# Kernel optimization log

Measured on AMD Instinct MI355X. Metric: run time of the kernel, lower is better.

## Reference

```python
import jax, jax.numpy as jnp
import numpy as np

N = 8192
F_IN = 128
F_OUT = 128


def setup_inputs() -> dict:
    key = jax.random.key(0)
    k1, k2, k3, k4, k5 = jax.random.split(key, 5)
    x = jax.random.normal(k1, (N, F_IN), dtype=jnp.float32)
    adj = jax.random.uniform(k2, (N, N), dtype=jnp.float32)
    kernel = jax.random.normal(k3, (F_IN, F_OUT), dtype=jnp.float32) * 0.05
    bias = jax.random.normal(k4, (F_OUT,), dtype=jnp.float32) * 0.05
    beta = jax.random.uniform(k5, (N,), dtype=jnp.float32)
    return {"x": x, "adj": adj, "kernel": kernel, "bias": bias, "beta": beta}


def reference(x, adj, kernel, bias, beta):
    # torch: diag(1/(adj.sum(1)+beta)) @ (adj + diag(beta)) @ x @ kernel + bias
    # (adj + diag(beta)) @ x  ==  adj @ x + beta[:, None] * x  (no NxN temp)
    inv_deg = 1.0 / (jnp.sum(adj, axis=1) + beta)        # [N]
    agg = adj @ x + beta[:, None] * x                     # [N, F_in]
    out = (inv_deg[:, None] * agg) @ kernel + bias        # [N, F_out]
    return out
```

## Files before the change

### kernel.cpp

```cpp
#include <hip/hip_runtime.h>

#define NN 8192
#define FD 128
#define BK 64
#define LDSR 72

typedef float f32x4 __attribute__((ext_vector_type(4)));
typedef short short8 __attribute__((ext_vector_type(8)));
typedef unsigned short ushort4v __attribute__((ext_vector_type(4)));
typedef unsigned short ushort8v __attribute__((ext_vector_type(8)));

__device__ __forceinline__ unsigned short f2bf(float f) {
  unsigned int u = __builtin_bit_cast(unsigned int, f);
  u += 0x7fffu + ((u >> 16) & 1u);
  return (unsigned short)(u >> 16);
}
__device__ __forceinline__ float bf2f(unsigned short h) {
  unsigned int u = ((unsigned int)h) << 16;
  return __builtin_bit_cast(float, u);
}

__global__ __launch_bounds__(256) void xk_kernel(
    const float* __restrict__ x, const float* __restrict__ kern,
    unsigned short* __restrict__ bfrag, unsigned short* __restrict__ xk_rm) {
  __shared__ __align__(16) unsigned short kl[FD * FD];
  __shared__ __align__(16) float xl[16 * FD];
  const int t = threadIdx.x;
  const int row0 = blockIdx.x * 16;

  #pragma unroll
  for (int j = 0; j < 16; ++j) {
    int idx = (j * 256 + t) * 4;
    f32x4 kv = *(const f32x4*)&kern[idx];
    ushort4v kw;
    #pragma unroll
    for (int q = 0; q < 4; ++q) kw[q] = f2bf(kv[q]);
    *(ushort4v*)&kl[idx] = kw;
  }
  #pragma unroll
  for (int j = 0; j < 2; ++j) {
    int idx = (j * 256 + t) * 4;
    *(f32x4*)&xl[idx] = *(const f32x4*)&x[(size_t)row0 * FD + idx];
  }
  __syncthreads();

  const int r0 = (t >> 5) * 2;
  const int c0 = (t & 31) * 4;
  float acc[2][4] = {};
  #pragma unroll 4
  for (int k = 0; k < FD; ++k) {
    ushort4v kq = *(const ushort4v*)&kl[k * FD + c0];
    float kv[4];
    #pragma unroll
    for (int q = 0; q < 4; ++q) kv[q] = bf2f(kq[q]);
    float x0 = xl[r0 * FD + k];
    float x1 = xl[(r0 + 1) * FD + k];
    #pragma unroll
    for (int q = 0; q < 4; ++q) {
      acc[0][q] += x0 * kv[q];
      acc[1][q] += x1 * kv[q];
    }
  }
  #pragma unroll
  for (int i = 0; i < 2; ++i) {
    const int r = row0 + r0 + i;
    const int kt = r >> 5;
    const int lhi = ((r >> 3) & 3) * 16;
    const int j = r & 7;
    ushort4v ow;
    #pragma unroll
    for (int q = 0; q < 4; ++q) {
      const int c = c0 + q;
      unsigned short bv = f2bf(acc[i][q]);
      ow[q] = bv;
      bfrag[(((size_t)kt * 8 + (c >> 4)) * 64 + (lhi + (c & 15))) * 8 + j] = bv;
    }
    *(ushort4v*)&xk_rm[(size_t)r * FD + c0] = ow;
  }
}

template <int S>
__global__ __launch_bounds__(256) void gcn_mm(
    const float* __restrict__ adj, const unsigned short* __restrict__ bfrag,
    unsigned short* __restrict__ parts, float* __restrict__ rowpart) {
  constexpr int KW = NN / S;
  constexpr int NS = KW / BK;
  __shared__ __align__(16) unsigned short sA[4][2][32 * LDSR];

  const int t = threadIdx.x;
  const int l = t & 63;
  const int w = t >> 6;
  const int b = blockIdx.x;
  const int s = b & (S - 1);
  const int row0 = (b / S) * 128 + w * 32;
  const int kbase = s * KW;

  const float* ap = adj + (size_t)(row0 + (l >> 4)) * NN + kbase + (l & 15) * 4;
  unsigned short* sw = &sA[w][0][0];
  const int wofs = (l >> 4) * LDSR + (l & 15) * 4;
  const unsigned short* bp = bfrag + (size_t)l * 8;

  f32x4 Lr[8];
  f32x4 acc[2][8] = {};
  float rs[8] = {0.f, 0.f, 0.f, 0.f, 0.f, 0.f, 0.f, 0.f};

  #pragma unroll
  for (int i = 0; i < 8; ++i)
    Lr[i] = *(const f32x4*)(ap + (size_t)i * 4 * NN);
  #pragma unroll
  for (int i = 0; i < 8; ++i) {
    ushort4v cw;
    #pragma unroll
    for (int q = 0; q < 4; ++q) cw[q] = f2bf(Lr[i][q]);
    rs[i] += Lr[i][0] + Lr[i][1] + Lr[i][2] + Lr[i][3];
    *(ushort4v*)&sw[wofs + i * 4 * LDSR] = cw;
  }

  #pragma unroll 2
  for (int st = 0; st < NS; ++st) {
    const int cur = st & 1;
    if (st + 1 < NS) {
      #pragma unroll
      for (int i = 0; i < 8; ++i)
        Lr[i] = *(const f32x4*)(ap + (size_t)i * 4 * NN + (st + 1) * BK);
    }
    const int ktg = s * (KW / 32) + st * 2;
    #pragma unroll
    for (int h = 0; h < 2; ++h) {
      const int abase = cur * 32 * LDSR + h * 32 + (l >> 4) * 8;
      short8 aF0 = *(const short8*)&sw[abase + (l & 15) * LDSR];
      short8 aF1 = *(const short8*)&sw[abase + (16 + (l & 15)) * LDSR];
      #pragma unroll
      for (int cb = 0; cb < 8; ++cb) {
        ushort8v Bf = *(const ushort8v*)(bp + (((size_t)(ktg + h) * 8 + cb) << 9));
        acc[0][cb] = __builtin_amdgcn_mfma_f32_16x16x32_bf16(aF0, Bf, acc[0][cb], 0, 0, 0);
        acc[1][cb] = __builtin_amdgcn_mfma_f32_16x16x32_bf16(aF1, Bf, acc[1][cb], 0, 0, 0);
      }
    }
    if (st + 1 < NS) {
      const int nb = (cur ^ 1) * 32 * LDSR;
      #pragma unroll
      for (int i = 0; i < 8; ++i) {
        ushort4v cw;
        #pragma unroll
        for (int q = 0; q < 4; ++q) cw[q] = f2bf(Lr[i][q]);
        rs[i] += Lr[i][0] + Lr[i][1] + Lr[i][2] + Lr[i][3];
        *(ushort4v*)&sw[nb + wofs + i * 4 * LDSR] = cw;
      }
    }
  }

  #pragma unroll
  for (int i = 0; i < 8; ++i) {
    rs[i] += __shfl_xor(rs[i], 1);
    rs[i] += __shfl_xor(rs[i], 2);
    rs[i] += __shfl_xor(rs[i], 4);
    rs[i] += __shfl_xor(rs[i], 8);
  }
  if ((l & 15) == 0) {
    #pragma unroll
    for (int i = 0; i < 8; ++i)
      rowpart[(size_t)s * NN + row0 + i * 4 + (l >> 4)] = rs[i];
  }

  unsigned short* pp = parts + ((size_t)s * NN + row0) * FD;
  #pragma unroll
  for (int rf = 0; rf < 2; ++rf)
    #pragma unroll
    for (int cb = 0; cb < 8; ++cb)
      #pragma unroll
      for (int j = 0; j < 4; ++j) {
        const int r = rf * 16 + ((l >> 4) << 2) + j;
        pp[(size_t)r * FD + cb * 16 + (l & 15)] = f2bf(acc[rf][cb][j]);
      }
}

__global__ __launch_bounds__(256) void gcn_fin(
    const unsigned short* __restrict__ parts, const float* __restrict__ rowpart,
    const unsigned short* __restrict__ xk_rm, const float* __restrict__ beta,
    const float* __restrict__ bias, float* __restrict__ out, int S) {
  const int t = threadIdx.x;
  const int r = blockIdx.x * 16 + (t >> 4);
  const int c0 = (t & 15) * 8;

  float rsum = 0.f;
  for (int s = 0; s < S; ++s) rsum += rowpart[(size_t)s * NN + r];
  const float bt = beta[r];
  const float inv = 1.0f / (rsum + bt);

  float a[8] = {0.f, 0.f, 0.f, 0.f, 0.f, 0.f, 0.f, 0.f};
  for (int s = 0; s < S; ++s) {
    ushort8v pv = *(const ushort8v*)&parts[((size_t)s * NN + r) * FD + c0];
    #pragma unroll
    for (int q = 0; q < 8; ++q) a[q] += bf2f(pv[q]);
  }
  ushort8v xv = *(const ushort8v*)&xk_rm[(size_t)r * FD + c0];
  f32x4 o0, o1;
  #pragma unroll
  for (int q = 0; q < 4; ++q) {
    o0[q] = (a[q] + bt * bf2f(xv[q])) * inv + bias[c0 + q];
    o1[q] = (a[4 + q] + bt * bf2f(xv[4 + q])) * inv + bias[c0 + 4 + q];
  }
  *(f32x4*)&out[(size_t)r * FD + c0] = o0;
  *(f32x4*)&out[(size_t)r * FD + c0 + 4] = o1;
}

extern "C" void kernel_launch(void* const* d_in, const int* in_sizes, int n_in,
                              void* d_out, int out_size, void* d_ws, size_t ws_size,
                              hipStream_t stream) {
  const float* x    = (const float*)d_in[0];
  const float* adj  = (const float*)d_in[1];
  const float* kern = (const float*)d_in[2];
  const float* bias = (const float*)d_in[3];
  const float* beta = (const float*)d_in[4];
  float* out = (float*)d_out;

  char* ws = (char*)d_ws;
  unsigned short* bfrag = (unsigned short*)ws;
  unsigned short* xk_rm = (unsigned short*)(ws + (size_t)NN * FD * 2);
  const size_t off_rowpart = (size_t)NN * FD * 4;
  float* rowpart = (float*)(ws + off_rowpart);
  const size_t off_parts = off_rowpart + (size_t)8 * NN * 4;
  unsigned short* parts = (unsigned short*)(ws + off_parts);

  int S = 8;
  while (S > 1 && off_parts + (size_t)S * NN * FD * 2 > ws_size) S >>= 1;

  hipLaunchKernelGGL(xk_kernel, dim3(NN / 16), dim3(256), 0, stream,
                     x, kern, bfrag, xk_rm);

  dim3 blk(256);
  switch (S) {
    case 8: hipLaunchKernelGGL(gcn_mm<8>, dim3(64 * 8), blk, 0, stream, adj, bfrag, parts, rowpart); break;
    case 4: hipLaunchKernelGGL(gcn_mm<4>, dim3(64 * 4), blk, 0, stream, adj, bfrag, parts, rowpart); break;
    case 2: hipLaunchKernelGGL(gcn_mm<2>, dim3(64 * 2), blk, 0, stream, adj, bfrag, parts, rowpart); break;
    default: hipLaunchKernelGGL(gcn_mm<1>, dim3(64), blk, 0, stream, adj, bfrag, parts, rowpart); break;
  }

  hipLaunchKernelGGL(gcn_fin, dim3(NN / 16), dim3(256), 0, stream,
                     parts, rowpart, xk_rm, beta, bias, out, S);
}
```

Measured before the change: 85.15 us.

## Deepen adj prefetch to two stages and batch B-fragment loads in gcn_mm

Restructures the gcn_mm main loop to double-buffer adj tiles in two register sets, so loads are issued two k-steps ahead. It also hoists all B-fragment global loads ahead of the MFMA block, raises wave priority with s_setprio around the MFMAs, and sets launch_bounds(256,2). The aim is to hide HBM latency on the adj stream and keep the matrix cores busy. The extra register arrays raise VGPR pressure and could cost occupancy or cause spills.

```diff
diff --git a/kernel.cpp b/kernel.cpp
--- a/kernel.cpp
+++ b/kernel.cpp
@@ -79,8 +79,47 @@
   }
 }
 
+#define PREFETCH(Lr, stp)                                                     \
+  do {                                                                        \
+    _Pragma("unroll") for (int i = 0; i < 8; ++i)                             \
+        Lr[i] = *(const f32x4*)(ap + (size_t)i * 4 * NN + (stp) * BK);        \
+  } while (0)
+
+#define STAGE(Lr, bufofs)                                                     \
+  do {                                                                        \
+    _Pragma("unroll") for (int i = 0; i < 8; ++i) {                           \
+      ushort4v cw;                                                            \
+      _Pragma("unroll") for (int q = 0; q < 4; ++q) cw[q] = f2bf(Lr[i][q]);   \
+      rs[i] += Lr[i][0] + Lr[i][1] + Lr[i][2] + Lr[i][3];                     \
+      *(ushort4v*)&sw[(bufofs) + wofs + i * 4 * LDSR] = cw;                   \
+    }                                                                         \
+  } while (0)
+
+#define MFMA_STEP(stp, bufofs)                                                \
+  do {                                                                        \
+    const int ktg = kt0 + (stp) * 2;                                          \
+    ushort8v Bf[2][8];                                                        \
+    _Pragma("unroll") for (int h = 0; h < 2; ++h)                             \
+        _Pragma("unroll") for (int cb = 0; cb < 8; ++cb)                      \
+            Bf[h][cb] = *(const ushort8v*)(bp +                               \
+                (((size_t)(ktg + h) * 8 + cb) << 9));                         \
+    __builtin_amdgcn_s_setprio(1);                                            \
+    _Pragma("unroll") for (int h = 0; h < 2; ++h) {                           \
+      const int abase = (bufofs) + h * 32 + (l >> 4) * 8;                     \
+      short8 aF0 = *(const short8*)&sw[abase + (l & 15) * LDSR];              \
+      short8 aF1 = *(const short8*)&sw[abase + (16 + (l & 15)) * LDSR];       \
+      _Pragma("unroll") for (int cb = 0; cb < 8; ++cb) {                      \
+        acc[0][cb] = __builtin_amdgcn_mfma_f32_16x16x32_bf16(                 \
+            aF0, Bf[h][cb], acc[0][cb], 0, 0, 0);                             \
+        acc[1][cb] = __builtin_amdgcn_mfma_f32_16x16x32_bf16(                 \
+            aF1, Bf[h][cb], acc[1][cb], 0, 0, 0);                             \
+      }                                                                       \
+    }                                                                         \
+    __builtin_amdgcn_s_setprio(0);                                            \
+  } while (0)
+
 template <int S>
-__global__ __launch_bounds__(256) void gcn_mm(
+__global__ __launch_bounds__(256, 2) void gcn_mm(
     const float* __restrict__ adj, const unsigned short* __restrict__ bfrag,
     unsigned short* __restrict__ parts, float* __restrict__ rowpart) {
   constexpr int KW = NN / S;
@@ -94,60 +133,29 @@
   const int s = b & (S - 1);
   const int row0 = (b / S) * 128 + w * 32;
   const int kbase = s * KW;
+  const int kt0 = s * (KW / 32);
 
   const float* ap = adj + (size_t)(row0 + (l >> 4)) * NN + kbase + (l & 15) * 4;
   unsigned short* sw = &sA[w][0][0];
   const int wofs = (l >> 4) * LDSR + (l & 15) * 4;
+  const int B1OFS = 32 * LDSR;
   const unsigned short* bp = bfrag + (size_t)l * 8;
 
-  f32x4 Lr[8];
+  f32x4 LrA[8], LrB[8];
   f32x4 acc[2][8] = {};
   float rs[8] = {0.f, 0.f, 0.f, 0.f, 0.f, 0.f, 0.f, 0.f};
 
-  #pragma unroll
-  for (int i = 0; i < 8; ++i)
-    Lr[i] = *(const f32x4*)(ap + (size_t)i * 4 * NN);
-  #pragma unroll
-  for (int i = 0; i < 8; ++i) {
-    ushort4v cw;
-    #pragma unroll
-    for (int q = 0; q < 4; ++q) cw[q] = f2bf(Lr[i][q]);
-    rs[i] += Lr[i][0] + Lr[i][1] + Lr[i][2] + Lr[i][3];
-    *(ushort4v*)&sw[wofs + i * 4 * LDSR] = cw;
-  }
-
-  #pragma unroll 2
-  for (int st = 0; st < NS; ++st) {
-    const int cur = st & 1;
-    if (st + 1 < NS) {
-      #pragma unroll
-      for (int i = 0; i < 8; ++i)
-        Lr[i] = *(const f32x4*)(ap + (size_t)i * 4 * NN + (st + 1) * BK);
-    }
-    const int ktg = s * (KW / 32) + st * 2;
-    #pragma unroll
-    for (int h = 0; h < 2; ++h) {
-      const int abase = cur * 32 * LDSR + h * 32 + (l >> 4) * 8;
-      short8 aF0 = *(const short8*)&sw[abase + (l & 15) * LDSR];
-      short8 aF1 = *(const short8*)&sw[abase + (16 + (l & 15)) * LDSR];
-      #pragma unroll
-      for (int cb = 0; cb < 8; ++cb) {
-        ushort8v Bf = *(const ushort8v*)(bp + (((size_t)(ktg + h) * 8 + cb) << 9));
-        acc[0][cb] = __builtin_amdgcn_mfma_f32_16x16x32_bf16(aF0, Bf, acc[0][cb], 0, 0, 0);
-        acc[1][cb] = __builtin_amdgcn_mfma_f32_16x16x32_bf16(aF1, Bf, acc[1][cb], 0, 0, 0);
-      }
-    }
-    if (st + 1 < NS) {
-      const int nb = (cur ^ 1) * 32 * LDSR;
-      #pragma unroll
-      for (int i = 0; i < 8; ++i) {
-        ushort4v cw;
-        #pragma unroll
-        for (int q = 0; q < 4; ++q) cw[q] = f2bf(Lr[i][q]);
-        rs[i] += Lr[i][0] + Lr[i][1] + Lr[i][2] + Lr[i][3];
-        *(ushort4v*)&sw[nb + wofs + i * 4 * LDSR] = cw;
-      }
-    }
+  PREFETCH(LrA, 0);
+  STAGE(LrA, 0);
+  PREFETCH(LrB, 1);
+
+  for (int st = 0; st < NS; st += 2) {
+    if (st + 2 < NS) PREFETCH(LrA, st + 2);
+    MFMA_STEP(st, 0);
+    STAGE(LrB, B1OFS);
+    if (st + 3 < NS) PREFETCH(LrB, st + 3);
+    MFMA_STEP(st + 1, B1OFS);
+    if (st + 2 < NS) STAGE(LrA, 0);
   }
 
   #pragma unroll
```

Result: faster. 83.40 us (-2.1%).

## Restructure adjacency GEMM into 32-row full-K panels with swizzled LDS and column-split waves

Applied to the files above, without the earlier changes.

Changes gcn_mm so each block loads a whole 32x1024 slice of adj into a swizzled 64KB LDS panel in one pass, instead of streaming 64-wide K tiles per wave with register double-buffering. The four waves then split the 128 output columns, 32 per wave, rather than splitting rows. This gives 2048 blocks with launch_bounds(256,2), trading the per-step load/compute overlap for more parallelism and occupancy. It also fixes the split count at 8 and drops the workspace-size fallback.

```diff
diff --git a/kernel.cpp b/kernel.cpp
--- a/kernel.cpp
+++ b/kernel.cpp
@@ -2,8 +2,10 @@
 
 #define NN 8192
 #define FD 128
-#define BK 64
-#define LDSR 72
+#define RPB 32
+#define SPL 8
+#define KW (NN / SPL)
+#define NKS (KW / 32)
 
 typedef float f32x4 __attribute__((ext_vector_type(4)));
 typedef short short8 __attribute__((ext_vector_type(8)));
@@ -79,117 +81,109 @@
   }
 }
 
-template <int S>
-__global__ __launch_bounds__(256) void gcn_mm(
+__global__ __launch_bounds__(256, 2) void gcn_mm(
     const float* __restrict__ adj, const unsigned short* __restrict__ bfrag,
     unsigned short* __restrict__ parts, float* __restrict__ rowpart) {
-  constexpr int KW = NN / S;
-  constexpr int NS = KW / BK;
-  __shared__ __align__(16) unsigned short sA[4][2][32 * LDSR];
+  __shared__ unsigned short panel[RPB * 1024];
+  __shared__ float rs_l[4][8];
 
   const int t = threadIdx.x;
   const int l = t & 63;
   const int w = t >> 6;
   const int b = blockIdx.x;
-  const int s = b & (S - 1);
-  const int row0 = (b / S) * 128 + w * 32;
+  const int s = b & (SPL - 1);
+  const int row0 = (b >> 3) * RPB;
   const int kbase = s * KW;
-
-  const float* ap = adj + (size_t)(row0 + (l >> 4)) * NN + kbase + (l & 15) * 4;
-  unsigned short* sw = &sA[w][0][0];
-  const int wofs = (l >> 4) * LDSR + (l & 15) * 4;
+  const int kt0 = s * NKS;
+
+  const float* ap = adj + (size_t)row0 * NN + kbase;
+  float rsum[8] = {};
+
+  #pragma unroll
+  for (int half = 0; half < 2; ++half) {
+    f32x4 v[16];
+    #pragma unroll
+    for (int i16 = 0; i16 < 16; ++i16) {
+      const int i = half * 16 + i16;
+      const int rr = i >> 2, ch = i & 3;
+      v[i16] = *(const f32x4*)(ap + (size_t)(w * 8 + rr) * NN + ch * 256 + l * 4);
+    }
+    #pragma unroll
+    for (int i16 = 0; i16 < 16; ++i16) {
+      const int i = half * 16 + i16;
+      const int rr = i >> 2, ch = i & 3;
+      const int row_l = w * 8 + rr;
+      ushort4v cw;
+      #pragma unroll
+      for (int q = 0; q < 4; ++q) cw[q] = f2bf(v[i16][q]);
+      rsum[rr] += v[i16][0] + v[i16][1] + v[i16][2] + v[i16][3];
+      const int unit = (ch * 32 + (l >> 1)) ^ (row_l & 7);
+      *(ushort4v*)&panel[row_l * 1024 + unit * 8 + (l & 1) * 4] = cw;
+    }
+  }
+
+  #pragma unroll
+  for (int rr = 0; rr < 8; ++rr) {
+    rsum[rr] += __shfl_xor(rsum[rr], 1);
+    rsum[rr] += __shfl_xor(rsum[rr], 2);
+    rsum[rr] += __shfl_xor(rsum[rr], 4);
+    rsum[rr] += __shfl_xor(rsum[rr], 8);
+    rsum[rr] += __shfl_xor(rsum[rr], 16);
+    rsum[rr] += __shfl_xor(rsum[rr], 32);
+  }
+  if (l == 0) {
+    #pragma unroll
+    for (int rr = 0; rr < 8; ++rr) rs_l[w][rr] = rsum[rr];
+  }
+  __syncthreads();
+
   const unsigned short* bp = bfrag + (size_t)l * 8;
-
-  f32x4 Lr[8];
-  f32x4 acc[2][8] = {};
-  float rs[8] = {0.f, 0.f, 0.f, 0.f, 0.f, 0.f, 0.f, 0.f};
-
-  #pragma unroll
-  for (int i = 0; i < 8; ++i)
-    Lr[i] = *(const f32x4*)(ap + (size_t)i * 4 * NN);
-  #pragma unroll
-  for (int i = 0; i < 8; ++i) {
-    ushort4v cw;
-    #pragma unroll
-    for (int q = 0; q < 4; ++q) cw[q] = f2bf(Lr[i][q]);
-    rs[i] += Lr[i][0] + Lr[i][1] + Lr[i][2] + Lr[i][3];
-    *(ushort4v*)&sw[wofs + i * 4 * LDSR] = cw;
-  }
-
-  #pragma unroll 2
-  for (int st = 0; st < NS; ++st) {
-    const int cur = st & 1;
-    if (st + 1 < NS) {
+  f32x4 acc[2][2] = {};
+
+  #pragma unroll 4
+  for (int ks = 0; ks < NKS; ++ks) {
+    ushort8v Bf0 = *(const ushort8v*)(bp + (((size_t)(kt0 + ks) * 8 + 2 * w) << 9));
+    ushort8v Bf1 = *(const ushort8v*)(bp + (((size_t)(kt0 + ks) * 8 + 2 * w + 1) << 9));
+    #pragma unroll
+    for (int mf = 0; mf < 2; ++mf) {
+      const int row = (l & 15) + 16 * mf;
+      const int unit = (ks * 4 + (l >> 4)) ^ (row & 7);
+      short8 aF = *(const short8*)&panel[row * 1024 + unit * 8];
+      acc[mf][0] = __builtin_amdgcn_mfma_f32_16x16x32_bf16(aF, Bf0, acc[mf][0], 0, 0, 0);
+      acc[mf][1] = __builtin_amdgcn_mfma_f32_16x16x32_bf16(aF, Bf1, acc[mf][1], 0, 0, 0);
+    }
+  }
+
+  if (t < RPB)
+    rowpart[(size_t)s * NN + row0 + t] = rs_l[t >> 3][t & 7];
+
+  unsigned short* pp = parts + ((size_t)s * NN + row0) * FD + w * 32;
+  #pragma unroll
+  for (int mf = 0; mf < 2; ++mf)
+    #pragma unroll
+    for (int ci = 0; ci < 2; ++ci)
       #pragma unroll
-      for (int i = 0; i < 8; ++i)
-        Lr[i] = *(const f32x4*)(ap + (size_t)i * 4 * NN + (st + 1) * BK);
-    }
-    const int ktg = s * (KW / 32) + st * 2;
-    #pragma unroll
-    for (int h = 0; h < 2; ++h) {
-      const int abase = cur * 32 * LDSR + h * 32 + (l >> 4) * 8;
-      short8 aF0 = *(const short8*)&sw[abase + (l & 15) * LDSR];
-      short8 aF1 = *(const short8*)&sw[abase + (16 + (l & 15)) * LDSR];
-      #pragma unroll
-      for (int cb = 0; cb < 8; ++cb) {
-        ushort8v Bf = *(const ushort8v*)(bp + (((size_t)(ktg + h) * 8 + cb) << 9));
-        acc[0][cb] = __builtin_amdgcn_mfma_f32_16x16x32_bf16(aF0, Bf, acc[0][cb], 0, 0, 0);
-        acc[1][cb] = __builtin_amdgcn_mfma_f32_16x16x32_bf16(aF1, Bf, acc[1][cb], 0, 0, 0);
-      }
-    }
-    if (st + 1 < NS) {
-      const int nb = (cur ^ 1) * 32 * LDSR;
-      #pragma unroll
-      for (int i = 0; i < 8; ++i) {
-        ushort4v cw;
-        #pragma unroll
-        for (int q = 0; q < 4; ++q) cw[q] = f2bf(Lr[i][q]);
-        rs[i] += Lr[i][0] + Lr[i][1] + Lr[i][2] + Lr[i][3];
-        *(ushort4v*)&sw[nb + wofs + i * 4 * LDSR] = cw;
-      }
-    }
-  }
-
-  #pragma unroll
-  for (int i = 0; i < 8; ++i) {
-    rs[i] += __shfl_xor(rs[i], 1);
-    rs[i] += __shfl_xor(rs[i], 2);
-    rs[i] += __shfl_xor(rs[i], 4);
-    rs[i] += __shfl_xor(rs[i], 8);
-  }
-  if ((l & 15) == 0) {
-    #pragma unroll
-    for (int i = 0; i < 8; ++i)
-      rowpart[(size_t)s * NN + row0 + i * 4 + (l >> 4)] = rs[i];
-  }
-
-  unsigned short* pp = parts + ((size_t)s * NN + row0) * FD;
-  #pragma unroll
-  for (int rf = 0; rf < 2; ++rf)
-    #pragma unroll
-    for (int cb = 0; cb < 8; ++cb)
-      #pragma unroll
-      for (int j = 0; j < 4; ++j) {
-        const int r = rf * 16 + ((l >> 4) << 2) + j;
-        pp[(size_t)r * FD + cb * 16 + (l & 15)] = f2bf(acc[rf][cb][j]);
+      for (int jj = 0; jj < 4; ++jj) {
+        const int r = mf * 16 + ((l >> 4) << 2) + jj;
+        pp[(size_t)r * FD + ci * 16 + (l & 15)] = f2bf(acc[mf][ci][jj]);
       }
 }
 
 __global__ __launch_bounds__(256) void gcn_fin(
     const unsigned short* __restrict__ parts, const float* __restrict__ rowpart,
     const unsigned short* __restrict__ xk_rm, const float* __restrict__ beta,
-    const float* __restrict__ bias, float* __restrict__ out, int S) {
+    const float* __restrict__ bias, float* __restrict__ out) {
   const int t = threadIdx.x;
   const int r = blockIdx.x * 16 + (t >> 4);
   const int c0 = (t & 15) * 8;
 
   float rsum = 0.f;
-  for (int s = 0; s < S; ++s) rsum += rowpart[(size_t)s * NN + r];
+  for (int s = 0; s < SPL; ++s) rsum += rowpart[(size_t)s * NN + r];
   const float bt = beta[r];
   const float inv = 1.0f / (rsum + bt);
 
   float a[8] = {0.f, 0.f, 0.f, 0.f, 0.f, 0.f, 0.f, 0.f};
-  for (int s = 0; s < S; ++s) {
+  for (int s = 0; s < SPL; ++s) {
     ushort8v pv = *(const ushort8v*)&parts[((size_t)s * NN + r) * FD + c0];
     #pragma unroll
     for (int q = 0; q < 8; ++q) a[q] += bf2f(pv[q]);
@@ -220,23 +214,13 @@
   unsigned short* xk_rm = (unsigned short*)(ws + (size_t)NN * FD * 2);
   const size_t off_rowpart = (size_t)NN * FD * 4;
   float* rowpart = (float*)(ws + off_rowpart);
-  const size_t off_parts = off_rowpart + (size_t)8 * NN * 4;
+  const size_t off_parts = off_rowpart + (size_t)SPL * NN * 4;
   unsigned short* parts = (unsigned short*)(ws + off_parts);
-
-  int S = 8;
-  while (S > 1 && off_parts + (size_t)S * NN * FD * 2 > ws_size) S >>= 1;
 
   hipLaunchKernelGGL(xk_kernel, dim3(NN / 16), dim3(256), 0, stream,
                      x, kern, bfrag, xk_rm);
-
-  dim3 blk(256);
-  switch (S) {
-    case 8: hipLaunchKernelGGL(gcn_mm<8>, dim3(64 * 8), blk, 0, stream, adj, bfrag, parts, rowpart); break;
-    case 4: hipLaunchKernelGGL(gcn_mm<4>, dim3(64 * 4), blk, 0, stream, adj, bfrag, parts, rowpart); break;
-    case 2: hipLaunchKernelGGL(gcn_mm<2>, dim3(64 * 2), blk, 0, stream, adj, bfrag, parts, rowpart); break;
-    default: hipLaunchKernelGGL(gcn_mm<1>, dim3(64), blk, 0, stream, adj, bfrag, parts, rowpart); break;
-  }
-
+  hipLaunchKernelGGL(gcn_mm, dim3((NN / RPB) * SPL), dim3(256), 0, stream,
+                     adj, bfrag, parts, rowpart);
   hipLaunchKernelGGL(gcn_fin, dim3(NN / 16), dim3(256), 0, stream,
-                     parts, rowpart, xk_rm, beta, bias, out, S);
-}
+                     parts, rowpart, xk_rm, beta, bias, out);
+}
```

Result: slower. 89.66 us (+5.3%).
